# Optimization experiments

Measured on AMD Instinct MI355X. Metric: run time of the kernel, lower is better.

The kernel has to match this reference:

```python
import jax, jax.numpy as jnp
import numpy as np

N_HEADS = 16

def setup_inputs() -> dict:
    key = jax.random.key(0)
    kx, kk, kq, kv, ko = jax.random.split(key, 5)
    B, T, D = 8, 1024, 1024
    s = 1.0 / np.sqrt(D)
    return {
        'x':  jax.random.normal(kx, (B, T, D), dtype=jnp.float32),
        'Wk': jax.random.normal(kk, (D, D), dtype=jnp.float32) * s,
        'Wq': jax.random.normal(kq, (D, D), dtype=jnp.float32) * s,
        'Wv': jax.random.normal(kv, (D, D), dtype=jnp.float32) * s,
        'Wo': jax.random.normal(ko, (D, D), dtype=jnp.float32) * s,
    }

def reference(x, Wk, Wq, Wv, Wo):
    B, T, D = x.shape
    H = D // N_HEADS  # head dim
    # projections (nn.Linear with bias=False: y = x @ W^T)
    k = (x @ Wk.T).reshape(B, T, N_HEADS, H).transpose(0, 2, 1, 3)  # [B,n,T,H]
    q = (x @ Wq.T).reshape(B, T, N_HEADS, H).transpose(0, 2, 1, 3)
    v = (x @ Wv.T).reshape(B, T, N_HEADS, H).transpose(0, 2, 1, 3)
    scores = jnp.einsum('bnqh,bnkh->bnqk', q, k)                    # [B,n,T,T]
    causal = jnp.tril(jnp.ones((T, T), dtype=bool))
    # original: masked_fill(-inf) BEFORE scaling; -inf/sqrt(H) stays -inf
    scores = jnp.where(causal, scores, -jnp.inf) / jnp.sqrt(jnp.float32(H))
    att = jax.nn.softmax(scores, axis=-1)
    # dropout p=0.0 -> identity
    out = jnp.einsum('bnqk,bnkh->bnqh', att, v)                     # [B,n,T,H]
    out = out.transpose(0, 2, 1, 3).reshape(B, T, D)
    return out @ Wo.T
```

## Files before the change

### kernel.cpp

```cpp
#include <hip/hip_runtime.h>
#include <stdint.h>

typedef __bf16 bf16x8 __attribute__((ext_vector_type(8)));
typedef float f32x4 __attribute__((ext_vector_type(4)));
typedef unsigned short ushort_t;
typedef unsigned int uint_t;

__device__ inline ushort_t f2bf(float f) {
  uint_t u = __builtin_bit_cast(uint_t, f);
  u = (u + 0x7FFFu + ((u >> 16) & 1u)) >> 16;
  return (ushort_t)u;
}

__device__ inline void gll16(const void* g, void* l) {
  __builtin_amdgcn_global_load_lds(
      (__attribute__((address_space(1))) void*)(uintptr_t)g,
      (__attribute__((address_space(3))) void*)(uint32_t)(uintptr_t)l,
      16, 0, 0);
}

__global__ void cast_bf16(const float* __restrict__ in, ushort_t* __restrict__ out,
                          int n4, float scale) {
  int i = blockIdx.x * blockDim.x + threadIdx.x;
  int st = gridDim.x * blockDim.x;
  for (; i < n4; i += st) {
    float4 v = reinterpret_cast<const float4*>(in)[i];
    ushort4 o;
    o.x = f2bf(v.x * scale);
    o.y = f2bf(v.y * scale);
    o.z = f2bf(v.z * scale);
    o.w = f2bf(v.w * scale);
    reinterpret_cast<ushort4*>(out)[i] = o;
  }
}

__global__ void cast_w4(const float* __restrict__ w0, const float* __restrict__ w1,
                        const float* __restrict__ w2, const float* __restrict__ w3,
                        ushort_t* __restrict__ out, float s0) {
  const int i = blockIdx.x * 256 + threadIdx.x;
  const int which = i >> 18;
  const float* src = which == 0 ? w0 : which == 1 ? w1 : which == 2 ? w2 : w3;
  const float sc = which == 0 ? s0 : 1.0f;
  float4 v = reinterpret_cast<const float4*>(src)[i & 0x3FFFF];
  ushort4 o;
  o.x = f2bf(v.x * sc);
  o.y = f2bf(v.y * sc);
  o.z = f2bf(v.z * sc);
  o.w = f2bf(v.w * sc);
  reinterpret_cast<ushort4*>(out)[i] = o;
}

#define MFMA16(A_, B_, C_) __builtin_amdgcn_mfma_f32_16x16x32_bf16(A_, B_, C_, 0, 0, 0)
#define SBAR __builtin_amdgcn_s_barrier
#define LGKM0 asm volatile("s_waitcnt lgkmcnt(0)" ::: "memory")

template <int MF, int NF, int NTN, int LDC, bool F32OUT>
__global__ __launch_bounds__(512, 2) void gemm8p(const ushort_t* __restrict__ A,
                                                 const ushort_t* __restrict__ B,
                                                 void* __restrict__ C) {
  constexpr int BM = MF * 32;
  constexpr int BN = NF * 64;
  constexpr int NA = BM / 64;
  constexpr int NB = BN / 64;
  constexpr int NB0 = 2;
  constexpr int NG0 = 2;
  constexpr int AU = BM * 64;
  constexpr int BUF = AU + BN * 64;
  constexpr int NWG = (8192 / BM) * NTN;
  __shared__ __attribute__((aligned(16))) ushort_t smem[2 * BUF];

  const int tid = threadIdx.x;
  const int lane = tid & 63;
  const int w = tid >> 6;
  const int wm = w >> 2, wn = w & 3;

  const int bid = blockIdx.x;
  const int swz = (bid & 7) * (NWG / 8) + (bid >> 3);
  const int m0 = (swz / NTN) * BM;
  const int n0 = (swz % NTN) * BN;

  const int scol = ((tid & 7) ^ ((tid >> 3) & 7)) * 8;
  const ushort_t* gA = A + (size_t)(m0 + (tid >> 3)) * 1024 + scol;
  const ushort_t* gB = B + (size_t)(n0 + (tid >> 3)) * 1024 + scol;

  const int lr = lane & 15;
  const int hi = lane >> 4;
  const int arow = (wm * MF * 16 + lr) * 64;
  const int brow = AU + (wn * NF * 16 + lr) * 64;
  const int cx0 = (hi * 8) ^ ((lane & 7) << 3);
  const int cx1 = cx0 ^ 32;

  f32x4 acc[MF][NF] = {};
  bf16x8 a[MF / 2][2];
  bf16x8 b[NF][2];

  auto stage_a_even = [&](int wbu, int sk) __attribute__((always_inline)) {
    if constexpr (MF == 8) {
      gll16(gA + 0 * 65536 + sk, &smem[wbu + 0 * 4096 + (w << 9)]);
      gll16(gA + 2 * 65536 + sk, &smem[wbu + 2 * 4096 + (w << 9)]);
    } else {
#pragma unroll
      for (int i = 0; i < NA; ++i)
        gll16(gA + i * 65536 + sk, &smem[wbu + i * 4096 + (w << 9)]);
    }
  };
  auto stage_a_odd = [&](int wbu, int sk) __attribute__((always_inline)) {
    if constexpr (MF == 8) {
      gll16(gA + 1 * 65536 + sk, &smem[wbu + 1 * 4096 + (w << 9)]);
      gll16(gA + 3 * 65536 + sk, &smem[wbu + 3 * 4096 + (w << 9)]);
    }
  };
  auto stage_b0 = [&](int wbu, int sk) __attribute__((always_inline)) {
#pragma unroll
    for (int i = 0; i < NB0; ++i)
      gll16(gB + i * 65536 + sk, &smem[wbu + AU + i * 4096 + (w << 9)]);
  };
  auto stage_b1 = [&](int wbu, int sk) __attribute__((always_inline)) {
#pragma unroll
    for (int i = NB0; i < NB; ++i)
      gll16(gB + i * 65536 + sk, &smem[wbu + AU + i * 4096 + (w << 9)]);
  };
  auto rdA = [&](int rbu, int mbase) __attribute__((always_inline)) {
#pragma unroll
    for (int m = 0; m < MF / 2; ++m) {
      const int base = rbu + arow + (mbase + m) * 1024;
      a[m][0] = *(const bf16x8*)&smem[base + cx0];
      a[m][1] = *(const bf16x8*)&smem[base + cx1];
    }
  };
  auto rdBg = [&](int rbu, int ng0, int ng1) __attribute__((always_inline)) {
#pragma unroll
    for (int n = 0; n < NF; ++n) {
      if (n < ng0 || n >= ng1) continue;
      const int base = rbu + brow + n * 1024;
      b[n][0] = *(const bf16x8*)&smem[base + cx0];
      b[n][1] = *(const bf16x8*)&smem[base + cx1];
    }
  };
  auto mmg = [&](int mbase, int ng0, int ng1) __attribute__((always_inline)) {
#pragma unroll
    for (int m = 0; m < MF / 2; ++m)
#pragma unroll
      for (int n = 0; n < NF; ++n) {
        if (n < ng0 || n >= ng1) continue;
        acc[mbase + m][n] = MFMA16(a[m][0], b[n][0], acc[mbase + m][n]);
        acc[mbase + m][n] = MFMA16(a[m][1], b[n][1], acc[mbase + m][n]);
      }
  };

  auto tile = [&](int rbu, int wbu, int sk, bool pf) __attribute__((always_inline)) {
    if (pf) {
      stage_a_even(wbu, sk);
      if constexpr (MF == 8)
        asm volatile("s_waitcnt vmcnt(4)" ::: "memory");
      else
        asm volatile("s_waitcnt vmcnt(2)" ::: "memory");
    } else {
      if constexpr (MF == 8)
        asm volatile("s_waitcnt vmcnt(2)" ::: "memory");
      else
        asm volatile("s_waitcnt vmcnt(0)" ::: "memory");
    }
    SBAR();
    rdA(rbu, 0);
    rdBg(rbu, 0, NG0);
    LGKM0;
    __builtin_amdgcn_s_setprio(1);
    mmg(0, 0, NG0);
    __builtin_amdgcn_s_setprio(0);
    SBAR();
    rdBg(rbu, NG0, NF);
    if (pf) stage_b0(wbu, sk);
    SBAR();
    LGKM0;
    __builtin_amdgcn_s_setprio(1);
    mmg(0, NG0, NF);
    __builtin_amdgcn_s_setprio(0);
    SBAR();
    if (pf) {
      stage_b1(wbu, sk);
      if constexpr (MF == 8)
        asm volatile("s_waitcnt vmcnt(5)" ::: "memory");
    } else {
      if constexpr (MF == 8)
        asm volatile("s_waitcnt vmcnt(0)" ::: "memory");
    }
    SBAR();
    rdA(rbu, MF / 2);
    LGKM0;
    __builtin_amdgcn_s_setprio(1);
    mmg(MF / 2, NG0, NF);
    __builtin_amdgcn_s_setprio(0);
    SBAR();
    if (pf) stage_a_odd(wbu, sk);
    SBAR();
    __builtin_amdgcn_s_setprio(1);
    mmg(MF / 2, 0, NG0);
    __builtin_amdgcn_s_setprio(0);
    SBAR();
  };

  stage_a_even(0, 0);
  stage_b0(0, 0);
  stage_b1(0, 0);
  stage_a_odd(0, 0);
  int sk = 64;
  for (int it = 0; it < 7; ++it) {
    tile(0, BUF, sk, true);
    sk += 64;
    tile(BUF, 0, sk, true);
    sk += 64;
  }
  tile(0, BUF, sk, true);
  tile(BUF, 0, 0, false);

  const size_t erow = (size_t)(m0 + wm * MF * 16 + hi * 4);
  const int ecol = n0 + wn * NF * 16 + lr;
#pragma unroll
  for (int mf = 0; mf < MF; ++mf)
#pragma unroll
    for (int nf = 0; nf < NF; ++nf)
#pragma unroll
      for (int r = 0; r < 4; ++r) {
        const size_t idx = (erow + mf * 16 + r) * LDC + ecol + nf * 16;
        if constexpr (F32OUT)
          ((float*)C)[idx] = acc[mf][nf][r];
        else
          ((ushort_t*)C)[idx] = f2bf(acc[mf][nf][r]);
      }
}

__global__ __launch_bounds__(256, 2) void attn_fwd(const ushort_t* __restrict__ QKV,
                                                   ushort_t* __restrict__ ctx) {
  const int bid = blockIdx.x;
  const int h = bid & 15;
  const int b = (bid >> 4) & 7;
  const int p = bid >> 7;
  const int tid = threadIdx.x;
  const int lane = tid & 63;
  const int w = tid >> 6;
  const int lr = lane & 15;
  const int lg = lane >> 4;
  const int dk = lg << 3;

  __shared__ __attribute__((aligned(16))) ushort_t Ks[2][64 * 72];
  __shared__ __attribute__((aligned(16))) uint_t VtDw[2][64 * 36];
  __shared__ __attribute__((aligned(16))) ushort_t Pl[4][32 * 72];

  const int kkey = tid >> 2, kdg = tid & 3;
  const int vkp = tid & 31, vdg = tid >> 5;
  const ushort_t* kgbase =
      QKV + ((size_t)(b * 1024 + kkey)) * 3072 + 1024 + h * 64 + kdg * 16;
  const ushort_t* vgbase =
      QKV + ((size_t)(b * 1024 + 2 * vkp)) * 3072 + 2048 + h * 64 + vdg * 8;

  const float FMAX2 = 23.083120654223414f;

  for (int pi = 0; pi < 2; ++pi) {
    const int qt = pi ? (7 - p) : p;
    const int q0 = qt << 7;
    const int nt = (qt + 1) << 1;
    const int wrow0 = q0 + w * 32;

    bf16x8 qf[2][2];
#pragma unroll
    for (int i = 0; i < 2; ++i) {
      const ushort_t* qp =
          QKV + ((size_t)(b * 1024 + wrow0 + i * 16 + lr)) * 3072 + h * 64 + dk;
      qf[i][0] = *reinterpret_cast<const bf16x8*>(qp);
      qf[i][1] = *reinterpret_cast<const bf16x8*>(qp + 32);
    }

    f32x4 o[2][4] = {};
    float lsum[2] = {0.f, 0.f};

    uint4 rk0 = *reinterpret_cast<const uint4*>(kgbase);
    uint4 rk1 = *reinterpret_cast<const uint4*>(kgbase + 8);
    uint4 rv0 = *reinterpret_cast<const uint4*>(vgbase);
    uint4 rv1 = *reinterpret_cast<const uint4*>(vgbase + 3072);

    for (int t = 0; t < nt; ++t) {
      const int bsel = t & 1;
      asm volatile("s_waitcnt vmcnt(0)" ::: "memory");
      {
        uint_t* kd = reinterpret_cast<uint_t*>(&Ks[bsel][kkey * 72 + kdg * 16]);
        *reinterpret_cast<uint4*>(kd) = rk0;
        *reinterpret_cast<uint4*>(kd + 4) = rk1;
        const ushort_t* e0 = reinterpret_cast<const ushort_t*>(&rv0);
        const ushort_t* e1 = reinterpret_cast<const ushort_t*>(&rv1);
#pragma unroll
        for (int j = 0; j < 8; ++j)
          VtDw[bsel][(vdg * 8 + j) * 36 + vkp] = (uint_t)e0[j] | ((uint_t)e1[j] << 16);
      }
      if (t + 1 < nt) {
        const size_t off = (size_t)(t + 1) * 64 * 3072;
        rk0 = *reinterpret_cast<const uint4*>(kgbase + off);
        rk1 = *reinterpret_cast<const uint4*>(kgbase + off + 8);
        rv0 = *reinterpret_cast<const uint4*>(vgbase + off);
        rv1 = *reinterpret_cast<const uint4*>(vgbase + off + 3072);
      }
      asm volatile("s_waitcnt lgkmcnt(0)" ::: "memory");
      __builtin_amdgcn_s_barrier();

      const int kb = t << 6;
      if (kb > wrow0 + 31) continue;

      bf16x8 kf0[4], kf1[4];
#pragma unroll
      for (int f = 0; f < 4; ++f) {
        kf0[f] = *reinterpret_cast<const bf16x8*>(&Ks[bsel][(f * 16 + lr) * 72 + dk]);
        kf1[f] =
            *reinterpret_cast<const bf16x8*>(&Ks[bsel][(f * 16 + lr) * 72 + 32 + dk]);
      }
      f32x4 s[2][4];
#pragma unroll
      for (int i = 0; i < 2; ++i)
#pragma unroll
        for (int f = 0; f < 4; ++f) {
          f32x4 z = {0.f, 0.f, 0.f, 0.f};
          z = __builtin_amdgcn_mfma_f32_16x16x32_bf16(kf0[f], qf[i][0], z, 0, 0, 0);
          s[i][f] = __builtin_amdgcn_mfma_f32_16x16x32_bf16(kf1[f], qf[i][1], z, 0, 0, 0);
        }

      const bool needmask = (kb + 63 > wrow0);
#pragma unroll
      for (int i = 0; i < 2; ++i) {
        const int qr = wrow0 + i * 16 + lr;
#pragma unroll
        for (int f = 0; f < 4; ++f) {
          const int kbase = kb + f * 16 + (lg << 2);
          float p0 = __builtin_amdgcn_exp2f(s[i][f][0] - FMAX2);
          float p1 = __builtin_amdgcn_exp2f(s[i][f][1] - FMAX2);
          float p2 = __builtin_amdgcn_exp2f(s[i][f][2] - FMAX2);
          float p3 = __builtin_amdgcn_exp2f(s[i][f][3] - FMAX2);
          if (needmask) {
            p0 = (kbase + 0 <= qr) ? p0 : 0.f;
            p1 = (kbase + 1 <= qr) ? p1 : 0.f;
            p2 = (kbase + 2 <= qr) ? p2 : 0.f;
            p3 = (kbase + 3 <= qr) ? p3 : 0.f;
          }
          lsum[i] += (p0 + p1) + (p2 + p3);
          ushort4 pk = {f2bf(p0), f2bf(p1), f2bf(p2), f2bf(p3)};
          *reinterpret_cast<ushort4*>(
              &Pl[w][(i * 16 + lr) * 72 + f * 16 + (lg << 2)]) = pk;
        }
      }

      bf16x8 vb[2][4];
#pragma unroll
      for (int kblk = 0; kblk < 2; ++kblk)
#pragma unroll
        for (int fh = 0; fh < 4; ++fh)
          vb[kblk][fh] = *reinterpret_cast<const bf16x8*>(
              &VtDw[bsel][(fh * 16 + lr) * 36 + kblk * 16 + (lg << 2)]);
#pragma unroll
      for (int i = 0; i < 2; ++i)
#pragma unroll
        for (int kblk = 0; kblk < 2; ++kblk) {
          const bf16x8 pa = *reinterpret_cast<const bf16x8*>(
              &Pl[w][(i * 16 + lr) * 72 + kblk * 32 + dk]);
#pragma unroll
          for (int fh = 0; fh < 4; ++fh)
            o[i][fh] = __builtin_amdgcn_mfma_f32_16x16x32_bf16(pa, vb[kblk][fh],
                                                               o[i][fh], 0, 0, 0);
        }
    }

#pragma unroll
    for (int i = 0; i < 2; ++i) {
      float ls = lsum[i];
      ls += __shfl_xor(ls, 16);
      ls += __shfl_xor(ls, 32);
      const float linv = 1.0f / ls;
      const size_t crow = (size_t)(b * 1024 + wrow0 + i * 16 + (lg << 2));
#pragma unroll
      for (int r = 0; r < 4; ++r) {
        const float li = __shfl(linv, (lg << 2) + r);
#pragma unroll
        for (int fh = 0; fh < 4; ++fh)
          ctx[(crow + r) * 1024 + h * 64 + fh * 16 + lr] = f2bf(o[i][fh][r] * li);
      }
    }
  }
}

extern "C" void kernel_launch(void* const* d_in, const int* in_sizes, int n_in,
                              void* d_out, int out_size, void* d_ws, size_t ws_size,
                              hipStream_t stream) {
  const float* x = (const float*)d_in[0];
  const float* Wk = (const float*)d_in[1];
  const float* Wq = (const float*)d_in[2];
  const float* Wv = (const float*)d_in[3];
  const float* Wo = (const float*)d_in[4];

  char* ws = (char*)d_ws;
  ushort_t* xb = (ushort_t*)ws;
  ushort_t* Wc = (ushort_t*)(ws + (16u << 20));
  ushort_t* Wob = Wc + 3u * 1024 * 1024;
  ushort_t* QKV = (ushort_t*)(ws + (24u << 20));
  ushort_t* ctx = xb;

  cast_bf16<<<2048, 256, 0, stream>>>(x, xb, (8192 * 1024) / 4, 1.0f);
  cast_w4<<<4096, 256, 0, stream>>>(Wq, Wk, Wv, Wo, Wc, 0.125f * 1.4426950408889634f);

  gemm8p<8, 3, 16, 3072, false><<<512, 512, 0, stream>>>(xb, Wc, QKV);

  attn_fwd<<<512, 256, 0, stream>>>(QKV, ctx);

  gemm8p<4, 4, 4, 1024, true><<<256, 512, 0, stream>>>(ctx, Wob, (float*)d_out);
}
```

Before: 135.8 us.

## Process both paired causal query tiles in one K/V sweep

Each block used to run two separate passes over the key/value tiles, one per paired query tile (p and 7-p). Now it makes a single pass up to the longer tile's range and computes both query groups against each K/V tile staged in LDS. This halves K/V global loads and LDS staging for the shared prefix and removes the barriers of the second pass. The cost is more live registers for two sets of Q fragments and accumulators. It also swaps the software bf16 rounding of P for the packed v_cvt_pk_bf16_f32 instruction.

```diff
diff --git a/kernel.cpp b/kernel.cpp
--- a/kernel.cpp
+++ b/kernel.cpp
@@ -256,62 +256,77 @@
 
   const float FMAX2 = 23.083120654223414f;
 
-  for (int pi = 0; pi < 2; ++pi) {
-    const int qt = pi ? (7 - p) : p;
-    const int q0 = qt << 7;
-    const int nt = (qt + 1) << 1;
-    const int wrow0 = q0 + w * 32;
-
-    bf16x8 qf[2][2];
-#pragma unroll
-    for (int i = 0; i < 2; ++i) {
-      const ushort_t* qp =
-          QKV + ((size_t)(b * 1024 + wrow0 + i * 16 + lr)) * 3072 + h * 64 + dk;
-      qf[i][0] = *reinterpret_cast<const bf16x8*>(qp);
-      qf[i][1] = *reinterpret_cast<const bf16x8*>(qp + 32);
-    }
-
-    f32x4 o[2][4] = {};
-    float lsum[2] = {0.f, 0.f};
-
-    uint4 rk0 = *reinterpret_cast<const uint4*>(kgbase);
-    uint4 rk1 = *reinterpret_cast<const uint4*>(kgbase + 8);
-    uint4 rv0 = *reinterpret_cast<const uint4*>(vgbase);
-    uint4 rv1 = *reinterpret_cast<const uint4*>(vgbase + 3072);
-
-    for (int t = 0; t < nt; ++t) {
-      const int bsel = t & 1;
-      asm volatile("s_waitcnt vmcnt(0)" ::: "memory");
-      {
-        uint_t* kd = reinterpret_cast<uint_t*>(&Ks[bsel][kkey * 72 + kdg * 16]);
-        *reinterpret_cast<uint4*>(kd) = rk0;
-        *reinterpret_cast<uint4*>(kd + 4) = rk1;
-        const ushort_t* e0 = reinterpret_cast<const ushort_t*>(&rv0);
-        const ushort_t* e1 = reinterpret_cast<const ushort_t*>(&rv1);
-#pragma unroll
-        for (int j = 0; j < 8; ++j)
-          VtDw[bsel][(vdg * 8 + j) * 36 + vkp] = (uint_t)e0[j] | ((uint_t)e1[j] << 16);
-      }
-      if (t + 1 < nt) {
-        const size_t off = (size_t)(t + 1) * 64 * 3072;
-        rk0 = *reinterpret_cast<const uint4*>(kgbase + off);
-        rk1 = *reinterpret_cast<const uint4*>(kgbase + off + 8);
-        rv0 = *reinterpret_cast<const uint4*>(vgbase + off);
-        rv1 = *reinterpret_cast<const uint4*>(vgbase + off + 3072);
-      }
-      asm volatile("s_waitcnt lgkmcnt(0)" ::: "memory");
-      __builtin_amdgcn_s_barrier();
-
-      const int kb = t << 6;
-      if (kb > wrow0 + 31) continue;
-
-      bf16x8 kf0[4], kf1[4];
-#pragma unroll
-      for (int f = 0; f < 4; ++f) {
-        kf0[f] = *reinterpret_cast<const bf16x8*>(&Ks[bsel][(f * 16 + lr) * 72 + dk]);
-        kf1[f] =
-            *reinterpret_cast<const bf16x8*>(&Ks[bsel][(f * 16 + lr) * 72 + 32 + dk]);
-      }
+  const int qtA = p, qtB = 7 - p;
+  const int ntB = (qtB + 1) << 1;
+  const int wrow0A = (qtA << 7) + w * 32;
+  const int wrow0B = (qtB << 7) + w * 32;
+
+  bf16x8 qfA[2][2], qfB[2][2];
+#pragma unroll
+  for (int i = 0; i < 2; ++i) {
+    const ushort_t* qpA =
+        QKV + ((size_t)(b * 1024 + wrow0A + i * 16 + lr)) * 3072 + h * 64 + dk;
+    qfA[i][0] = *reinterpret_cast<const bf16x8*>(qpA);
+    qfA[i][1] = *reinterpret_cast<const bf16x8*>(qpA + 32);
+    const ushort_t* qpB =
+        QKV + ((size_t)(b * 1024 + wrow0B + i * 16 + lr)) * 3072 + h * 64 + dk;
+    qfB[i][0] = *reinterpret_cast<const bf16x8*>(qpB);
+    qfB[i][1] = *reinterpret_cast<const bf16x8*>(qpB + 32);
+  }
+
+  f32x4 oA[2][4] = {}, oB[2][4] = {};
+  float lsA[2] = {0.f, 0.f}, lsB[2] = {0.f, 0.f};
+
+  uint4 rk0 = *reinterpret_cast<const uint4*>(kgbase);
+  uint4 rk1 = *reinterpret_cast<const uint4*>(kgbase + 8);
+  uint4 rv0 = *reinterpret_cast<const uint4*>(vgbase);
+  uint4 rv1 = *reinterpret_cast<const uint4*>(vgbase + 3072);
+
+  for (int t = 0; t < ntB; ++t) {
+    const int bsel = t & 1;
+    asm volatile("s_waitcnt vmcnt(0)" ::: "memory");
+    {
+      uint_t* kd = reinterpret_cast<uint_t*>(&Ks[bsel][kkey * 72 + kdg * 16]);
+      *reinterpret_cast<uint4*>(kd) = rk0;
+      *reinterpret_cast<uint4*>(kd + 4) = rk1;
+      const ushort_t* e0 = reinterpret_cast<const ushort_t*>(&rv0);
+      const ushort_t* e1 = reinterpret_cast<const ushort_t*>(&rv1);
+#pragma unroll
+      for (int j = 0; j < 8; ++j)
+        VtDw[bsel][(vdg * 8 + j) * 36 + vkp] = (uint_t)e0[j] | ((uint_t)e1[j] << 16);
+    }
+    if (t + 1 < ntB) {
+      const size_t off = (size_t)(t + 1) * 64 * 3072;
+      rk0 = *reinterpret_cast<const uint4*>(kgbase + off);
+      rk1 = *reinterpret_cast<const uint4*>(kgbase + off + 8);
+      rv0 = *reinterpret_cast<const uint4*>(vgbase + off);
+      rv1 = *reinterpret_cast<const uint4*>(vgbase + off + 3072);
+    }
+    asm volatile("s_waitcnt lgkmcnt(0)" ::: "memory");
+    __builtin_amdgcn_s_barrier();
+
+    const int kb = t << 6;
+    const bool actB = (kb <= wrow0B + 31);
+    const bool actA = (kb <= wrow0A + 31);
+    if (!(actA || actB)) continue;
+
+    bf16x8 kf0[4], kf1[4];
+#pragma unroll
+    for (int f = 0; f < 4; ++f) {
+      kf0[f] = *reinterpret_cast<const bf16x8*>(&Ks[bsel][(f * 16 + lr) * 72 + dk]);
+      kf1[f] =
+          *reinterpret_cast<const bf16x8*>(&Ks[bsel][(f * 16 + lr) * 72 + 32 + dk]);
+    }
+    bf16x8 vb[2][4];
+#pragma unroll
+    for (int kblk = 0; kblk < 2; ++kblk)
+#pragma unroll
+      for (int fh = 0; fh < 4; ++fh)
+        vb[kblk][fh] = *reinterpret_cast<const bf16x8*>(
+            &VtDw[bsel][(fh * 16 + lr) * 36 + kblk * 16 + (lg << 2)]);
+
+    auto group = [&](const bf16x8(&qf)[2][2], f32x4(&o)[2][4], float(&ls)[2],
+                     int wrow0) __attribute__((always_inline)) {
       f32x4 s[2][4];
 #pragma unroll
       for (int i = 0; i < 2; ++i)
@@ -321,7 +336,6 @@
           z = __builtin_amdgcn_mfma_f32_16x16x32_bf16(kf0[f], qf[i][0], z, 0, 0, 0);
           s[i][f] = __builtin_amdgcn_mfma_f32_16x16x32_bf16(kf1[f], qf[i][1], z, 0, 0, 0);
         }
-
       const bool needmask = (kb + 63 > wrow0);
 #pragma unroll
       for (int i = 0; i < 2; ++i) {
@@ -339,20 +353,15 @@
             p2 = (kbase + 2 <= qr) ? p2 : 0.f;
             p3 = (kbase + 3 <= qr) ? p3 : 0.f;
           }
-          lsum[i] += (p0 + p1) + (p2 + p3);
-          ushort4 pk = {f2bf(p0), f2bf(p1), f2bf(p2), f2bf(p3)};
-          *reinterpret_cast<ushort4*>(
+          ls[i] += (p0 + p1) + (p2 + p3);
+          uint_t q01, q23;
+          asm("v_cvt_pk_bf16_f32 %0, %1, %2" : "=v"(q01) : "v"(p0), "v"(p1));
+          asm("v_cvt_pk_bf16_f32 %0, %1, %2" : "=v"(q23) : "v"(p2), "v"(p3));
+          uint2 pk = {q01, q23};
+          *reinterpret_cast<uint2*>(
               &Pl[w][(i * 16 + lr) * 72 + f * 16 + (lg << 2)]) = pk;
         }
       }
-
-      bf16x8 vb[2][4];
-#pragma unroll
-      for (int kblk = 0; kblk < 2; ++kblk)
-#pragma unroll
-        for (int fh = 0; fh < 4; ++fh)
-          vb[kblk][fh] = *reinterpret_cast<const bf16x8*>(
-              &VtDw[bsel][(fh * 16 + lr) * 36 + kblk * 16 + (lg << 2)]);
 #pragma unroll
       for (int i = 0; i < 2; ++i)
 #pragma unroll
@@ -364,14 +373,20 @@
             o[i][fh] = __builtin_amdgcn_mfma_f32_16x16x32_bf16(pa, vb[kblk][fh],
                                                                o[i][fh], 0, 0, 0);
         }
-    }
-
+    };
+
+    if (actB) group(qfB, oB, lsB, wrow0B);
+    if (actA) group(qfA, oA, lsA, wrow0A);
+  }
+
+  auto epi = [&](f32x4(&o)[2][4], float(&ls)[2], int wrow0)
+      __attribute__((always_inline)) {
 #pragma unroll
     for (int i = 0; i < 2; ++i) {
-      float ls = lsum[i];
-      ls += __shfl_xor(ls, 16);
-      ls += __shfl_xor(ls, 32);
-      const float linv = 1.0f / ls;
+      float s = ls[i];
+      s += __shfl_xor(s, 16);
+      s += __shfl_xor(s, 32);
+      const float linv = 1.0f / s;
       const size_t crow = (size_t)(b * 1024 + wrow0 + i * 16 + (lg << 2));
 #pragma unroll
       for (int r = 0; r < 4; ++r) {
@@ -381,7 +396,9 @@
           ctx[(crow + r) * 1024 + h * 64 + fh * 16 + lr] = f2bf(o[i][fh][r] * li);
       }
     }
-  }
+  };
+  epi(oB, lsB, wrow0B);
+  epi(oA, lsA, wrow0A);
 }
 
 extern "C" void kernel_launch(void* const* d_in, const int* in_sizes, int n_in,
```

Result: faster. 131.5 us (-3.2%).
